# Performance work log

Measured on AMD Instinct MI355X. Metric: run time of the kernel, lower is better.

Reference implementation:

```python
import jax, jax.numpy as jnp
import numpy as np

NEG = -1000000.0  # same finite mask value as the Triton kernel


def setup_inputs() -> dict:
    key = jax.random.key(0)
    k1, k2, k3, k4 = jax.random.split(key, 4)
    B, H, KVH, S, D = 1, 32, 8, 2048, 128
    return {
        "q": jax.random.normal(k1, (B, H, S, D), dtype=jnp.float32),
        "k": jax.random.normal(k2, (B, KVH, S, D), dtype=jnp.float32),
        "v": jax.random.normal(k3, (B, KVH, S, D), dtype=jnp.float32),
        "sinks": jax.random.normal(k4, (H,), dtype=jnp.float32),
        "bandwidth": 1024,
    }


def reference(q, k, v, sinks, bandwidth):
    """Prefill flash attention with causal + sliding-window masking, GQA, and
    per-head attention sinks (extra logit in the softmax denominator)."""
    B, H, S, D = q.shape
    ratio = H // k.shape[1]  # KV_HEAD_RATIO
    kf = jnp.repeat(k, ratio, axis=1)  # [B,H,S,D]
    vf = jnp.repeat(v, ratio, axis=1)
    sm_scale = 1.0 / np.sqrt(D).astype(np.float32)

    logits = jnp.einsum("bhqd,bhkd->bhqk", q, kf) * sm_scale  # [B,H,S,S]
    q_pos = jnp.arange(S)[:, None]
    k_pos = jnp.arange(S)[None, :]
    mask = k_pos > q_pos  # causal
    if bandwidth > 0:
        mask = mask | (k_pos < q_pos - bandwidth + 1)  # sliding window
    logits = jnp.where(mask, NEG, logits)

    sink = sinks[None, :, None]  # [1,H,1] broadcast over batch, query
    m = jnp.maximum(jnp.max(logits, axis=-1), sink)  # [B,H,S]
    p = jnp.exp(logits - m[..., None])
    denom = p.sum(axis=-1) + jnp.exp(sink - m)  # sink contributes to denom only
    out = jnp.einsum("bhqk,bhkd->bhqd", p, vf) / denom[..., None]
    return out
```

## Files before the change

kernel.cpp:

```cpp
#include <hip/hip_runtime.h>
#include <hip/hip_bf16.h>

typedef __bf16 bf16x8 __attribute__((ext_vector_type(8)));
typedef unsigned short u16x8 __attribute__((ext_vector_type(8)));
typedef unsigned int u32x4 __attribute__((ext_vector_type(4)));
typedef float f32x4 __attribute__((ext_vector_type(4)));

#define SLEN 2048
#define DDIM 128
#define NH   32
#define NKVH 8
#define QBLK 128
#define KVB  32
#define KPAD 136
#define VPAD 40
#define PW2  20
#define MINIT  -1e30f
#define MASKED -3e30f

static __device__ __forceinline__ unsigned short f2bfu(float f) {
  union { float f; unsigned u; } x; x.f = f;
  return (unsigned short)((x.u + 0x7fffu + ((x.u >> 16) & 1u)) >> 16);
}
static __device__ __forceinline__ float bfu2f(unsigned short u) {
  union { unsigned u; float f; } x; x.u = ((unsigned)u) << 16;
  return x.f;
}
static __device__ __forceinline__ unsigned cvt_pk_bf16(float lo, float hi) {
  unsigned r;
  asm("v_cvt_pk_bf16_f32 %0, %1, %2" : "=v"(r) : "v"(lo), "v"(hi));
  return r;
}
static __device__ __forceinline__ f32x4 mfma_bf16(u16x8 a, u16x8 b, f32x4 c) {
  return __builtin_amdgcn_mfma_f32_16x16x32_bf16(
      __builtin_bit_cast(bf16x8, a), __builtin_bit_cast(bf16x8, b), c, 0, 0, 0);
}

__global__ __launch_bounds__(256) void conv_kv(const float* __restrict__ k,
                                               const float* __restrict__ v,
                                               unsigned* __restrict__ kdst,
                                               unsigned short* __restrict__ vt) {
  __shared__ unsigned T32[32][17];
  const int bb = blockIdx.x;
  if (bb < 1024) {
    const int i = bb * 256 + threadIdx.x;
    const float4 f0 = ((const float4*)k)[2 * i];
    const float4 f1 = ((const float4*)k)[2 * i + 1];
    u32x4 o = { cvt_pk_bf16(f0.x, f0.y), cvt_pk_bf16(f0.z, f0.w),
                cvt_pk_bf16(f1.x, f1.y), cvt_pk_bf16(f1.z, f1.w) };
    ((u32x4*)kdst)[i] = o;
    return;
  }
  const int b   = bb - 1024;
  const int dt  = b & 3;
  const int st  = (b >> 2) & 63;
  const int kvh = b >> 8;
  const int r  = threadIdx.x >> 3;
  const int cg = threadIdx.x & 7;
  const float4 f = *(const float4*)(v + ((size_t)(kvh * SLEN + st * 32 + r) * DDIM) + dt * 32 + cg * 4);
  T32[r][cg * 2]     = cvt_pk_bf16(f.x, f.y);
  T32[r][cg * 2 + 1] = cvt_pk_bf16(f.z, f.w);
  __syncthreads();
  const int dr = threadIdx.x >> 3;
  const unsigned sel = (dr & 1) ? 0x07060302u : 0x05040100u;
  const unsigned a0 = T32[cg * 4 + 0][dr >> 1], a1 = T32[cg * 4 + 1][dr >> 1];
  const unsigned a2 = T32[cg * 4 + 2][dr >> 1], a3 = T32[cg * 4 + 3][dr >> 1];
  unsigned short* vp = vt + (size_t)kvh * DDIM * SLEN + (size_t)(dt * 32 + dr) * SLEN + st * 32 + cg * 4;
  const unsigned w0 = __builtin_amdgcn_perm(a1, a0, sel);
  const unsigned w1 = __builtin_amdgcn_perm(a3, a2, sel);
  vp[0] = (unsigned short)(w0 & 0xffff);
  vp[1] = (unsigned short)(w0 >> 16);
  vp[2] = (unsigned short)(w1 & 0xffff);
  vp[3] = (unsigned short)(w1 >> 16);
}

__global__ __launch_bounds__(256, 3) void attn_fwd(
    const float* __restrict__ q, const unsigned short* __restrict__ kbf,
    const unsigned short* __restrict__ vtg, const float* __restrict__ sinks,
    const int* __restrict__ bwp, float* __restrict__ out,
    unsigned short* __restrict__ pO, float* __restrict__ pm,
    float* __restrict__ pl, const int nch) {
  __shared__ unsigned short Kl[KVB][KPAD];
  __shared__ unsigned short Vt[DDIM][VPAD];
  __shared__ unsigned Pex[4][2][16][PW2];
  __shared__ float SmS[4][2][16];

  const int tid  = threadIdx.x;
  const int wid  = tid >> 6;
  const int lane = tid & 63;
  const int ln   = lane & 15;
  const int hi   = lane >> 4;

  const int B   = blockIdx.x;
  const int x   = B & 7;
  const int j   = B >> 3;
  const int per = 4 * nch;
  const int qt  = 15 - (j / per);
  const int rem = j % per;
  const int hh  = (nch == 2) ? (rem >> 1) : rem;
  const int c   = (nch == 2) ? (rem & 1) : 0;
  const int h   = x * 4 + hh;
  const int kvh = x;
  const int q0  = qt * QBLK;
  const int qrow0 = q0 + wid * 32;

  const int bwv    = bwp[0];
  const int lo_off = (bwv > 0) ? (bwv - 1) : SLEN;

  const int T0 = max(0, q0 - lo_off) >> 5;
  const int T1 = (q0 + QBLK - 1) >> 5;
  const int N  = T1 - T0 + 1;
  const int ch = (N + nch - 1) / nch;
  const int Ts = T0 + c * ch;
  const int Te = min(T1, Ts + ch - 1);

  const float sm_scale = 0.08838834764831845f;

  u16x8 qf[2][4];
  #pragma unroll
  for (int g = 0; g < 2; ++g) {
    const float* qp = q + ((size_t)(h * SLEN + qrow0 + g * 16 + ln) * DDIM) + hi * 8;
    #pragma unroll
    for (int dk = 0; dk < 4; ++dk) {
      float4 f0 = *(const float4*)(qp + dk * 32);
      float4 f1 = *(const float4*)(qp + dk * 32 + 4);
      u32x4 t = { cvt_pk_bf16(f0.x, f0.y), cvt_pk_bf16(f0.z, f0.w),
                  cvt_pk_bf16(f1.x, f1.y), cvt_pk_bf16(f1.z, f1.w) };
      qf[g][dk] = __builtin_bit_cast(u16x8, t);
    }
  }

  float m[2] = {MINIT, MINIT}, l[2] = {0.0f, 0.0f};
  f32x4 oacc[2][8];
  #pragma unroll
  for (int g = 0; g < 2; ++g)
    #pragma unroll
    for (int nt = 0; nt < 8; ++nt) oacc[g][nt] = f32x4{0.f, 0.f, 0.f, 0.f};

  const unsigned short* Kg = kbf + (size_t)kvh * SLEN * DDIM;
  const unsigned short* Vg = vtg + (size_t)kvh * DDIM * SLEN;

  const int kr0 = tid >> 4,          kc0 = (tid & 15) * 8;
  const int kr1 = (256 + tid) >> 4;
  const int vr0 = tid >> 2,          vc0 = (tid & 3) * 8;
  const int vr1 = (256 + tid) >> 2;

  const int kbS = Ts * 32, kbE = Te * 32;

  u16x8 pk0, pk1, pv0, pv1;
  {
    pk0 = *(const u16x8*)(Kg + (size_t)(kbS + kr0) * DDIM + kc0);
    pk1 = *(const u16x8*)(Kg + (size_t)(kbS + kr1) * DDIM + kc0);
    pv0 = *(const u16x8*)(Vg + (size_t)vr0 * SLEN + kbS + vc0);
    pv1 = *(const u16x8*)(Vg + (size_t)vr1 * SLEN + kbS + vc0);
  }

  for (int kb = kbS; kb <= kbE; kb += KVB) {
    __syncthreads();
    *(u16x8*)&Kl[kr0][kc0] = pk0;
    *(u16x8*)&Kl[kr1][kc0] = pk1;
    *(u16x8*)&Vt[vr0][vc0] = pv0;
    *(u16x8*)&Vt[vr1][vc0] = pv1;
    __syncthreads();

    {
      const int nb = min(kb + KVB, kbE);
      pk0 = *(const u16x8*)(Kg + (size_t)(nb + kr0) * DDIM + kc0);
      pk1 = *(const u16x8*)(Kg + (size_t)(nb + kr1) * DDIM + kc0);
      pv0 = *(const u16x8*)(Vg + (size_t)vr0 * SLEN + nb + vc0);
      pv1 = *(const u16x8*)(Vg + (size_t)vr1 * SLEN + nb + vc0);
    }

    if (kb > qrow0 + 31) continue;
    if (kb + KVB - 1 < qrow0 - lo_off) continue;

    f32x4 s00 = {0,0,0,0}, s01 = {0,0,0,0};
    f32x4 s10 = {0,0,0,0}, s11 = {0,0,0,0};
    #pragma unroll
    for (int dk = 0; dk < 4; ++dk) {
      const u16x8 kf = *(const u16x8*)&Kl[ln][dk*32 + hi*8];
      s00 = mfma_bf16(kf, qf[0][dk], s00);
      s01 = mfma_bf16(kf, qf[1][dk], s01);
    }
    #pragma unroll
    for (int dk = 0; dk < 4; ++dk) {
      const u16x8 kf = *(const u16x8*)&Kl[16 + ln][dk*32 + hi*8];
      s10 = mfma_bf16(kf, qf[0][dk], s10);
      s11 = mfma_bf16(kf, qf[1][dk], s11);
    }

    float p0[8], p1[8];
    const int qpos0 = qrow0 + ln, qpos1 = qrow0 + 16 + ln;
    #pragma unroll
    for (int r = 0; r < 4; ++r) {
      const int kp0 = kb + hi * 4 + r;
      const int kp1 = kp0 + 16;
      p0[r]     = ((kp0 <= qpos0) && (kp0 >= qpos0 - lo_off)) ? s00[r] * sm_scale : MASKED;
      p0[4 + r] = ((kp1 <= qpos0) && (kp1 >= qpos0 - lo_off)) ? s10[r] * sm_scale : MASKED;
      p1[r]     = ((kp0 <= qpos1) && (kp0 >= qpos1 - lo_off)) ? s01[r] * sm_scale : MASKED;
      p1[4 + r] = ((kp1 <= qpos1) && (kp1 >= qpos1 - lo_off)) ? s11[r] * sm_scale : MASKED;
    }

    float mx0 = fmaxf(fmaxf(fmaxf(p0[0], p0[1]), fmaxf(p0[2], p0[3])),
                      fmaxf(fmaxf(p0[4], p0[5]), fmaxf(p0[6], p0[7])));
    float mx1 = fmaxf(fmaxf(fmaxf(p1[0], p1[1]), fmaxf(p1[2], p1[3])),
                      fmaxf(fmaxf(p1[4], p1[5]), fmaxf(p1[6], p1[7])));
    mx0 = fmaxf(mx0, __shfl_xor(mx0, 16));
    mx0 = fmaxf(mx0, __shfl_xor(mx0, 32));
    mx1 = fmaxf(mx1, __shfl_xor(mx1, 16));
    mx1 = fmaxf(mx1, __shfl_xor(mx1, 32));

    if (__any((mx0 > m[0] + 8.0f) || (mx1 > m[1] + 8.0f))) {
      const float mn0 = fmaxf(m[0], mx0), mn1 = fmaxf(m[1], mx1);
      const float c0 = __expf(m[0] - mn0), c1 = __expf(m[1] - mn1);
      l[0] *= c0; l[1] *= c1; m[0] = mn0; m[1] = mn1;
      if (hi == 0) { SmS[wid][0][ln] = c0; SmS[wid][1][ln] = c1; }
      float c40[4], c41[4];
      #pragma unroll
      for (int r = 0; r < 4; ++r) { c40[r] = SmS[wid][0][hi*4 + r]; c41[r] = SmS[wid][1][hi*4 + r]; }
      #pragma unroll
      for (int nt = 0; nt < 8; ++nt)
        #pragma unroll
        for (int r = 0; r < 4; ++r) { oacc[0][nt][r] *= c40[r]; oacc[1][nt][r] *= c41[r]; }
    }

    float s0 = 0.0f, s1 = 0.0f;
    #pragma unroll
    for (int jj = 0; jj < 8; ++jj) {
      p0[jj] = __expf(p0[jj] - m[0]); s0 += p0[jj];
      p1[jj] = __expf(p1[jj] - m[1]); s1 += p1[jj];
    }
    s0 += __shfl_xor(s0, 16); s0 += __shfl_xor(s0, 32); l[0] += s0;
    s1 += __shfl_xor(s1, 16); s1 += __shfl_xor(s1, 32); l[1] += s1;

    Pex[wid][0][ln][hi * 2]         = cvt_pk_bf16(p0[0], p0[1]);
    Pex[wid][0][ln][hi * 2 + 1]     = cvt_pk_bf16(p0[2], p0[3]);
    Pex[wid][0][ln][8 + hi * 2]     = cvt_pk_bf16(p0[4], p0[5]);
    Pex[wid][0][ln][8 + hi * 2 + 1] = cvt_pk_bf16(p0[6], p0[7]);
    Pex[wid][1][ln][hi * 2]         = cvt_pk_bf16(p1[0], p1[1]);
    Pex[wid][1][ln][hi * 2 + 1]     = cvt_pk_bf16(p1[2], p1[3]);
    Pex[wid][1][ln][8 + hi * 2]     = cvt_pk_bf16(p1[4], p1[5]);
    Pex[wid][1][ln][8 + hi * 2 + 1] = cvt_pk_bf16(p1[6], p1[7]);
    const u16x8 pa0 = __builtin_bit_cast(u16x8, *(const u32x4*)&Pex[wid][0][ln][hi * 4]);
    const u16x8 pa1 = __builtin_bit_cast(u16x8, *(const u32x4*)&Pex[wid][1][ln][hi * 4]);

    #pragma unroll
    for (int nt = 0; nt < 8; ++nt) {
      const u16x8 vb = *(const u16x8*)&Vt[nt*16 + ln][hi*8];
      oacc[0][nt] = mfma_bf16(pa0, vb, oacc[0][nt]);
      oacc[1][nt] = mfma_bf16(pa1, vb, oacc[1][nt]);
    }
  }

  if (nch == 1) {
    const float sink = sinks[h];
    #pragma unroll
    for (int g = 0; g < 2; ++g) {
      const float M  = fmaxf(m[g], sink);
      const float ed = __expf(m[g] - M);
      const float fac_ln = ed / (l[g] * ed + __expf(sink - M));
      if (hi == 0) SmS[wid][g][ln] = fac_ln;
      float fac4[4];
      #pragma unroll
      for (int r = 0; r < 4; ++r) fac4[r] = SmS[wid][g][hi * 4 + r];
      #pragma unroll
      for (int r = 0; r < 4; ++r) {
        float* op = out + ((size_t)(h * SLEN + qrow0 + g*16 + hi*4 + r) * DDIM) + ln;
        #pragma unroll
        for (int nt = 0; nt < 8; ++nt) op[nt * 16] = oacc[g][nt][r] * fac4[r];
      }
    }
  } else {
    const size_t Lb = ((size_t)(h * 16 + qt)) * 2 + c;
    #pragma unroll
    for (int g = 0; g < 2; ++g) {
      if (hi == 0) {
        pm[Lb * 128 + wid * 32 + g * 16 + ln] = m[g];
        pl[Lb * 128 + wid * 32 + g * 16 + ln] = l[g];
      }
      #pragma unroll
      for (int r = 0; r < 4; ++r) {
        unsigned short* po = pO + (Lb * 128 + wid * 32 + g * 16 + hi * 4 + r) * 128 + ln;
        #pragma unroll
        for (int nt = 0; nt < 8; ++nt) po[nt * 16] = f2bfu(oacc[g][nt][r]);
      }
    }
  }
}

__global__ __launch_bounds__(256) void merge2(
    const unsigned short* __restrict__ pO, const float* __restrict__ pm,
    const float* __restrict__ pl, const float* __restrict__ sinks,
    float* __restrict__ out) {
  const int blk  = blockIdx.x;
  const int h    = blk >> 5;
  const int rloc = (blk & 31) * 64 + (threadIdx.x >> 2);
  const int d0   = (threadIdx.x & 3) * 32;
  const int qt   = rloc >> 7;
  const int lr   = rloc & 127;
  const size_t r0 = ((size_t)((h * 16 + qt) * 2 + 0)) * 128 + lr;
  const size_t r1 = r0 + 128;
  const float m0 = pm[r0], l0 = pl[r0];
  const float m1 = pm[r1], l1 = pl[r1];
  const float sink = sinks[h];
  const float M  = fmaxf(fmaxf(m0, m1), sink);
  const float e0 = __expf(m0 - M), e1 = __expf(m1 - M);
  const float inv = 1.0f / (l0 * e0 + l1 * e1 + __expf(sink - M));
  const float s0 = e0 * inv, s1 = e1 * inv;
  const unsigned short* p0 = pO + r0 * 128 + d0;
  const unsigned short* p1 = pO + r1 * 128 + d0;
  float* op = out + ((size_t)h * SLEN + rloc) * DDIM + d0;
  #pragma unroll
  for (int i = 0; i < 4; ++i) {
    u16x8 a = *(const u16x8*)(p0 + i * 8);
    u16x8 b = *(const u16x8*)(p1 + i * 8);
    float4 o0, o1;
    o0.x = bfu2f(a[0]) * s0 + bfu2f(b[0]) * s1;
    o0.y = bfu2f(a[1]) * s0 + bfu2f(b[1]) * s1;
    o0.z = bfu2f(a[2]) * s0 + bfu2f(b[2]) * s1;
    o0.w = bfu2f(a[3]) * s0 + bfu2f(b[3]) * s1;
    o1.x = bfu2f(a[4]) * s0 + bfu2f(b[4]) * s1;
    o1.y = bfu2f(a[5]) * s0 + bfu2f(b[5]) * s1;
    o1.z = bfu2f(a[6]) * s0 + bfu2f(b[6]) * s1;
    o1.w = bfu2f(a[7]) * s0 + bfu2f(b[7]) * s1;
    *(float4*)(op + i * 8)     = o0;
    *(float4*)(op + i * 8 + 4) = o1;
  }
}

extern "C" void kernel_launch(void* const* d_in, const int* in_sizes, int n_in,
                              void* d_out, int out_size, void* d_ws, size_t ws_size,
                              hipStream_t stream) {
  const float* q     = (const float*)d_in[0];
  const float* k     = (const float*)d_in[1];
  const float* v     = (const float*)d_in[2];
  const float* sinks = (const float*)d_in[3];
  const int*   bw    = (const int*)d_in[4];
  float* out = (float*)d_out;

  const size_t kvBytes = (size_t)NKVH * SLEN * DDIM * 2;
  unsigned short* kbf = (unsigned short*)d_ws;
  unsigned short* vtg = kbf + (size_t)NKVH * SLEN * DDIM;

  const size_t nPart   = (size_t)NH * 16 * 2 * 128;
  const size_t oBytes  = nPart * 128 * 2;
  const size_t mlBytes = nPart * 4 * 2;
  const size_t need2   = 2 * kvBytes + oBytes + mlBytes;

  const int nch = (ws_size >= need2) ? 2 : 1;

  unsigned short* pO = vtg + (size_t)NKVH * SLEN * DDIM;
  float* pm = (float*)((char*)pO + oBytes);
  float* pl = pm + nPart;

  conv_kv<<<dim3(1024 + NKVH * 64 * 4), 256, 0, stream>>>(k, v, (unsigned*)kbf, vtg);
  attn_fwd<<<dim3(512 * nch), 256, 0, stream>>>(q, kbf, vtg, sinks, bw, out,
                                                pO, pm, pl, nch);
  if (nch == 2)
    merge2<<<dim3(1024), 256, 0, stream>>>(pO, pm, pl, sinks, out);
}
```

Measured before the change: 86.84 us.

## Template attention kernel on query groups and KV splits, add 4-way split path

The attention kernel is templated on the number of 16-row query groups per wave and the number of KV-range chunks. The default path (large workspace) splits each query tile's KV range into 4 chunks, launching 2048 blocks instead of 1024. A generic N-way merge kernel combines the partials. Fallbacks use 64-row query tiles with 2 chunks, or no split. This raises parallelism and load balance across CUs, at the cost of more partial-output traffic in bf16 and a heavier merge.

Result: slower. 109.2 us (+25.7%).

```diff
diff --git a/kernel.cpp b/kernel.cpp
--- a/kernel.cpp
+++ b/kernel.cpp
@@ -10,7 +10,6 @@
 #define DDIM 128
 #define NH   32
 #define NKVH 8
-#define QBLK 128
 #define KVB  32
 #define KPAD 136
 #define VPAD 40
@@ -74,16 +73,19 @@
   vp[3] = (unsigned short)(w1 >> 16);
 }
 
-__global__ __launch_bounds__(256, 3) void attn_fwd(
+template <int NG, int NCH>
+__global__ __launch_bounds__(256, NG == 1 ? 4 : 3) void attn_fwd(
     const float* __restrict__ q, const unsigned short* __restrict__ kbf,
     const unsigned short* __restrict__ vtg, const float* __restrict__ sinks,
     const int* __restrict__ bwp, float* __restrict__ out,
     unsigned short* __restrict__ pO, float* __restrict__ pm,
-    float* __restrict__ pl, const int nch) {
+    float* __restrict__ pl) {
+  constexpr int QBLK = 64 * NG;
+  constexpr int NQT  = SLEN / QBLK;
   __shared__ unsigned short Kl[KVB][KPAD];
   __shared__ unsigned short Vt[DDIM][VPAD];
-  __shared__ unsigned Pex[4][2][16][PW2];
-  __shared__ float SmS[4][2][16];
+  __shared__ unsigned Pex[4][16][PW2];
+  __shared__ float SmS[4][NG][16];
 
   const int tid  = threadIdx.x;
   const int wid  = tid >> 6;
@@ -94,15 +96,15 @@
   const int B   = blockIdx.x;
   const int x   = B & 7;
   const int j   = B >> 3;
-  const int per = 4 * nch;
-  const int qt  = 15 - (j / per);
+  constexpr int per = 4 * NCH;
+  const int qt  = NQT - 1 - (j / per);
   const int rem = j % per;
-  const int hh  = (nch == 2) ? (rem >> 1) : rem;
-  const int c   = (nch == 2) ? (rem & 1) : 0;
+  const int hh  = rem / NCH;
+  const int c   = rem % NCH;
   const int h   = x * 4 + hh;
   const int kvh = x;
   const int q0  = qt * QBLK;
-  const int qrow0 = q0 + wid * 32;
+  const int qrow0 = q0 + wid * (16 * NG);
 
   const int bwv    = bwp[0];
   const int lo_off = (bwv > 0) ? (bwv - 1) : SLEN;
@@ -110,15 +112,15 @@
   const int T0 = max(0, q0 - lo_off) >> 5;
   const int T1 = (q0 + QBLK - 1) >> 5;
   const int N  = T1 - T0 + 1;
-  const int ch = (N + nch - 1) / nch;
+  const int ch = (N + NCH - 1) / NCH;
   const int Ts = T0 + c * ch;
   const int Te = min(T1, Ts + ch - 1);
 
   const float sm_scale = 0.08838834764831845f;
 
-  u16x8 qf[2][4];
-  #pragma unroll
-  for (int g = 0; g < 2; ++g) {
+  u16x8 qf[NG][4];
+  #pragma unroll
+  for (int g = 0; g < NG; ++g) {
     const float* qp = q + ((size_t)(h * SLEN + qrow0 + g * 16 + ln) * DDIM) + hi * 8;
     #pragma unroll
     for (int dk = 0; dk < 4; ++dk) {
@@ -130,12 +132,14 @@
     }
   }
 
-  float m[2] = {MINIT, MINIT}, l[2] = {0.0f, 0.0f};
-  f32x4 oacc[2][8];
-  #pragma unroll
-  for (int g = 0; g < 2; ++g)
+  float m[NG], l[NG];
+  f32x4 oacc[NG][8];
+  #pragma unroll
+  for (int g = 0; g < NG; ++g) {
+    m[g] = MINIT; l[g] = 0.0f;
     #pragma unroll
     for (int nt = 0; nt < 8; ++nt) oacc[g][nt] = f32x4{0.f, 0.f, 0.f, 0.f};
+  }
 
   const unsigned short* Kg = kbf + (size_t)kvh * SLEN * DDIM;
   const unsigned short* Vg = vtg + (size_t)kvh * DDIM * SLEN;
@@ -145,117 +149,131 @@
   const int vr0 = tid >> 2,          vc0 = (tid & 3) * 8;
   const int vr1 = (256 + tid) >> 2;
 
-  const int kbS = Ts * 32, kbE = Te * 32;
-
-  u16x8 pk0, pk1, pv0, pv1;
-  {
-    pk0 = *(const u16x8*)(Kg + (size_t)(kbS + kr0) * DDIM + kc0);
-    pk1 = *(const u16x8*)(Kg + (size_t)(kbS + kr1) * DDIM + kc0);
-    pv0 = *(const u16x8*)(Vg + (size_t)vr0 * SLEN + kbS + vc0);
-    pv1 = *(const u16x8*)(Vg + (size_t)vr1 * SLEN + kbS + vc0);
-  }
-
-  for (int kb = kbS; kb <= kbE; kb += KVB) {
-    __syncthreads();
-    *(u16x8*)&Kl[kr0][kc0] = pk0;
-    *(u16x8*)&Kl[kr1][kc0] = pk1;
-    *(u16x8*)&Vt[vr0][vc0] = pv0;
-    *(u16x8*)&Vt[vr1][vc0] = pv1;
-    __syncthreads();
-
+  if (Ts <= Te) {
+    const int kbS = Ts * 32, kbE = Te * 32;
+
+    u16x8 pk0, pk1, pv0, pv1;
     {
-      const int nb = min(kb + KVB, kbE);
-      pk0 = *(const u16x8*)(Kg + (size_t)(nb + kr0) * DDIM + kc0);
-      pk1 = *(const u16x8*)(Kg + (size_t)(nb + kr1) * DDIM + kc0);
-      pv0 = *(const u16x8*)(Vg + (size_t)vr0 * SLEN + nb + vc0);
-      pv1 = *(const u16x8*)(Vg + (size_t)vr1 * SLEN + nb + vc0);
-    }
-
-    if (kb > qrow0 + 31) continue;
-    if (kb + KVB - 1 < qrow0 - lo_off) continue;
-
-    f32x4 s00 = {0,0,0,0}, s01 = {0,0,0,0};
-    f32x4 s10 = {0,0,0,0}, s11 = {0,0,0,0};
-    #pragma unroll
-    for (int dk = 0; dk < 4; ++dk) {
-      const u16x8 kf = *(const u16x8*)&Kl[ln][dk*32 + hi*8];
-      s00 = mfma_bf16(kf, qf[0][dk], s00);
-      s01 = mfma_bf16(kf, qf[1][dk], s01);
-    }
-    #pragma unroll
-    for (int dk = 0; dk < 4; ++dk) {
-      const u16x8 kf = *(const u16x8*)&Kl[16 + ln][dk*32 + hi*8];
-      s10 = mfma_bf16(kf, qf[0][dk], s10);
-      s11 = mfma_bf16(kf, qf[1][dk], s11);
-    }
-
-    float p0[8], p1[8];
-    const int qpos0 = qrow0 + ln, qpos1 = qrow0 + 16 + ln;
-    #pragma unroll
-    for (int r = 0; r < 4; ++r) {
-      const int kp0 = kb + hi * 4 + r;
-      const int kp1 = kp0 + 16;
-      p0[r]     = ((kp0 <= qpos0) && (kp0 >= qpos0 - lo_off)) ? s00[r] * sm_scale : MASKED;
-      p0[4 + r] = ((kp1 <= qpos0) && (kp1 >= qpos0 - lo_off)) ? s10[r] * sm_scale : MASKED;
-      p1[r]     = ((kp0 <= qpos1) && (kp0 >= qpos1 - lo_off)) ? s01[r] * sm_scale : MASKED;
-      p1[4 + r] = ((kp1 <= qpos1) && (kp1 >= qpos1 - lo_off)) ? s11[r] * sm_scale : MASKED;
-    }
-
-    float mx0 = fmaxf(fmaxf(fmaxf(p0[0], p0[1]), fmaxf(p0[2], p0[3])),
-                      fmaxf(fmaxf(p0[4], p0[5]), fmaxf(p0[6], p0[7])));
-    float mx1 = fmaxf(fmaxf(fmaxf(p1[0], p1[1]), fmaxf(p1[2], p1[3])),
-                      fmaxf(fmaxf(p1[4], p1[5]), fmaxf(p1[6], p1[7])));
-    mx0 = fmaxf(mx0, __shfl_xor(mx0, 16));
-    mx0 = fmaxf(mx0, __shfl_xor(mx0, 32));
-    mx1 = fmaxf(mx1, __shfl_xor(mx1, 16));
-    mx1 = fmaxf(mx1, __shfl_xor(mx1, 32));
-
-    if (__any((mx0 > m[0] + 8.0f) || (mx1 > m[1] + 8.0f))) {
-      const float mn0 = fmaxf(m[0], mx0), mn1 = fmaxf(m[1], mx1);
-      const float c0 = __expf(m[0] - mn0), c1 = __expf(m[1] - mn1);
-      l[0] *= c0; l[1] *= c1; m[0] = mn0; m[1] = mn1;
-      if (hi == 0) { SmS[wid][0][ln] = c0; SmS[wid][1][ln] = c1; }
-      float c40[4], c41[4];
-      #pragma unroll
-      for (int r = 0; r < 4; ++r) { c40[r] = SmS[wid][0][hi*4 + r]; c41[r] = SmS[wid][1][hi*4 + r]; }
-      #pragma unroll
-      for (int nt = 0; nt < 8; ++nt)
-        #pragma unroll
-        for (int r = 0; r < 4; ++r) { oacc[0][nt][r] *= c40[r]; oacc[1][nt][r] *= c41[r]; }
-    }
-
-    float s0 = 0.0f, s1 = 0.0f;
-    #pragma unroll
-    for (int jj = 0; jj < 8; ++jj) {
-      p0[jj] = __expf(p0[jj] - m[0]); s0 += p0[jj];
-      p1[jj] = __expf(p1[jj] - m[1]); s1 += p1[jj];
-    }
-    s0 += __shfl_xor(s0, 16); s0 += __shfl_xor(s0, 32); l[0] += s0;
-    s1 += __shfl_xor(s1, 16); s1 += __shfl_xor(s1, 32); l[1] += s1;
-
-    Pex[wid][0][ln][hi * 2]         = cvt_pk_bf16(p0[0], p0[1]);
-    Pex[wid][0][ln][hi * 2 + 1]     = cvt_pk_bf16(p0[2], p0[3]);
-    Pex[wid][0][ln][8 + hi * 2]     = cvt_pk_bf16(p0[4], p0[5]);
-    Pex[wid][0][ln][8 + hi * 2 + 1] = cvt_pk_bf16(p0[6], p0[7]);
-    Pex[wid][1][ln][hi * 2]         = cvt_pk_bf16(p1[0], p1[1]);
-    Pex[wid][1][ln][hi * 2 + 1]     = cvt_pk_bf16(p1[2], p1[3]);
-    Pex[wid][1][ln][8 + hi * 2]     = cvt_pk_bf16(p1[4], p1[5]);
-    Pex[wid][1][ln][8 + hi * 2 + 1] = cvt_pk_bf16(p1[6], p1[7]);
-    const u16x8 pa0 = __builtin_bit_cast(u16x8, *(const u32x4*)&Pex[wid][0][ln][hi * 4]);
-    const u16x8 pa1 = __builtin_bit_cast(u16x8, *(const u32x4*)&Pex[wid][1][ln][hi * 4]);
-
-    #pragma unroll
-    for (int nt = 0; nt < 8; ++nt) {
-      const u16x8 vb = *(const u16x8*)&Vt[nt*16 + ln][hi*8];
-      oacc[0][nt] = mfma_bf16(pa0, vb, oacc[0][nt]);
-      oacc[1][nt] = mfma_bf16(pa1, vb, oacc[1][nt]);
-    }
-  }
-
-  if (nch == 1) {
+      pk0 = *(const u16x8*)(Kg + (size_t)(kbS + kr0) * DDIM + kc0);
+      pk1 = *(const u16x8*)(Kg + (size_t)(kbS + kr1) * DDIM + kc0);
+      pv0 = *(const u16x8*)(Vg + (size_t)vr0 * SLEN + kbS + vc0);
+      pv1 = *(const u16x8*)(Vg + (size_t)vr1 * SLEN + kbS + vc0);
+    }
+
+    for (int kb = kbS; kb <= kbE; kb += KVB) {
+      __syncthreads();
+      *(u16x8*)&Kl[kr0][kc0] = pk0;
+      *(u16x8*)&Kl[kr1][kc0] = pk1;
+      *(u16x8*)&Vt[vr0][vc0] = pv0;
+      *(u16x8*)&Vt[vr1][vc0] = pv1;
+      __syncthreads();
+
+      {
+        const int nb = min(kb + KVB, kbE);
+        pk0 = *(const u16x8*)(Kg + (size_t)(nb + kr0) * DDIM + kc0);
+        pk1 = *(const u16x8*)(Kg + (size_t)(nb + kr1) * DDIM + kc0);
+        pv0 = *(const u16x8*)(Vg + (size_t)vr0 * SLEN + nb + vc0);
+        pv1 = *(const u16x8*)(Vg + (size_t)vr1 * SLEN + nb + vc0);
+      }
+
+      if (kb > qrow0 + 16 * NG - 1) continue;
+      if (kb + KVB - 1 < qrow0 - lo_off) continue;
+
+      f32x4 sA[NG], sB[NG];
+      #pragma unroll
+      for (int g = 0; g < NG; ++g) { sA[g] = f32x4{0,0,0,0}; sB[g] = f32x4{0,0,0,0}; }
+      #pragma unroll
+      for (int dk = 0; dk < 4; ++dk) {
+        const u16x8 kf = *(const u16x8*)&Kl[ln][dk*32 + hi*8];
+        #pragma unroll
+        for (int g = 0; g < NG; ++g) sA[g] = mfma_bf16(kf, qf[g][dk], sA[g]);
+      }
+      #pragma unroll
+      for (int dk = 0; dk < 4; ++dk) {
+        const u16x8 kf = *(const u16x8*)&Kl[16 + ln][dk*32 + hi*8];
+        #pragma unroll
+        for (int g = 0; g < NG; ++g) sB[g] = mfma_bf16(kf, qf[g][dk], sB[g]);
+      }
+
+      float p[NG][8];
+      #pragma unroll
+      for (int g = 0; g < NG; ++g) {
+        const int qpos = qrow0 + g * 16 + ln;
+        #pragma unroll
+        for (int r = 0; r < 4; ++r) {
+          const int kp0 = kb + hi * 4 + r;
+          const int kp1 = kp0 + 16;
+          p[g][r]     = ((kp0 <= qpos) && (kp0 >= qpos - lo_off)) ? sA[g][r] * sm_scale : MASKED;
+          p[g][4 + r] = ((kp1 <= qpos) && (kp1 >= qpos - lo_off)) ? sB[g][r] * sm_scale : MASKED;
+        }
+      }
+
+      float mx[NG];
+      bool need = false;
+      #pragma unroll
+      for (int g = 0; g < NG; ++g) {
+        float t = fmaxf(fmaxf(fmaxf(p[g][0], p[g][1]), fmaxf(p[g][2], p[g][3])),
+                        fmaxf(fmaxf(p[g][4], p[g][5]), fmaxf(p[g][6], p[g][7])));
+        t = fmaxf(t, __shfl_xor(t, 16));
+        t = fmaxf(t, __shfl_xor(t, 32));
+        mx[g] = t;
+        need = need || (t > m[g] + 8.0f);
+      }
+
+      if (__any(need)) {
+        float corr[NG];
+        #pragma unroll
+        for (int g = 0; g < NG; ++g) {
+          const float mn = fmaxf(m[g], mx[g]);
+          corr[g] = __expf(m[g] - mn);
+          l[g] *= corr[g];
+          m[g] = mn;
+          if (hi == 0) SmS[wid][g][ln] = corr[g];
+        }
+        #pragma unroll
+        for (int g = 0; g < NG; ++g) {
+          float c4[4];
+          #pragma unroll
+          for (int r = 0; r < 4; ++r) c4[r] = SmS[wid][g][hi * 4 + r];
+          #pragma unroll
+          for (int nt = 0; nt < 8; ++nt)
+            #pragma unroll
+            for (int r = 0; r < 4; ++r) oacc[g][nt][r] *= c4[r];
+        }
+      }
+
+      #pragma unroll
+      for (int g = 0; g < NG; ++g) {
+        float s = 0.0f;
+        #pragma unroll
+        for (int jj = 0; jj < 8; ++jj) { p[g][jj] = __expf(p[g][jj] - m[g]); s += p[g][jj]; }
+        s += __shfl_xor(s, 16);
+        s += __shfl_xor(s, 32);
+        l[g] += s;
+      }
+
+      u16x8 pa[NG];
+      #pragma unroll
+      for (int g = 0; g < NG; ++g) {
+        Pex[wid][ln][hi * 2]         = cvt_pk_bf16(p[g][0], p[g][1]);
+        Pex[wid][ln][hi * 2 + 1]     = cvt_pk_bf16(p[g][2], p[g][3]);
+        Pex[wid][ln][8 + hi * 2]     = cvt_pk_bf16(p[g][4], p[g][5]);
+        Pex[wid][ln][8 + hi * 2 + 1] = cvt_pk_bf16(p[g][6], p[g][7]);
+        pa[g] = __builtin_bit_cast(u16x8, *(const u32x4*)&Pex[wid][ln][hi * 4]);
+      }
+      #pragma unroll
+      for (int nt = 0; nt < 8; ++nt) {
+        const u16x8 vb = *(const u16x8*)&Vt[nt*16 + ln][hi*8];
+        #pragma unroll
+        for (int g = 0; g < NG; ++g) oacc[g][nt] = mfma_bf16(pa[g], vb, oacc[g][nt]);
+      }
+    }
+  }
+
+  if (NCH == 1) {
     const float sink = sinks[h];
     #pragma unroll
-    for (int g = 0; g < 2; ++g) {
+    for (int g = 0; g < NG; ++g) {
       const float M  = fmaxf(m[g], sink);
       const float ed = __expf(m[g] - M);
       const float fac_ln = ed / (l[g] * ed + __expf(sink - M));
@@ -271,16 +289,17 @@
       }
     }
   } else {
-    const size_t Lb = ((size_t)(h * 16 + qt)) * 2 + c;
-    #pragma unroll
-    for (int g = 0; g < 2; ++g) {
+    const size_t Lb = ((size_t)(h * NQT + qt)) * NCH + c;
+    #pragma unroll
+    for (int g = 0; g < NG; ++g) {
+      const int rbase = wid * (16 * NG) + g * 16;
       if (hi == 0) {
-        pm[Lb * 128 + wid * 32 + g * 16 + ln] = m[g];
-        pl[Lb * 128 + wid * 32 + g * 16 + ln] = l[g];
+        pm[Lb * QBLK + rbase + ln] = m[g];
+        pl[Lb * QBLK + rbase + ln] = l[g];
       }
       #pragma unroll
       for (int r = 0; r < 4; ++r) {
-        unsigned short* po = pO + (Lb * 128 + wid * 32 + g * 16 + hi * 4 + r) * 128 + ln;
+        unsigned short* po = pO + (Lb * QBLK + rbase + hi * 4 + r) * 128 + ln;
         #pragma unroll
         for (int nt = 0; nt < 8; ++nt) po[nt * 16] = f2bfu(oacc[g][nt][r]);
       }
@@ -288,44 +307,51 @@
   }
 }
 
-__global__ __launch_bounds__(256) void merge2(
+template <int NCH, int QBLK, int NQT>
+__global__ __launch_bounds__(256) void mergeN(
     const unsigned short* __restrict__ pO, const float* __restrict__ pm,
     const float* __restrict__ pl, const float* __restrict__ sinks,
     float* __restrict__ out) {
-  const int blk  = blockIdx.x;
-  const int h    = blk >> 5;
-  const int rloc = (blk & 31) * 64 + (threadIdx.x >> 2);
-  const int d0   = (threadIdx.x & 3) * 32;
-  const int qt   = rloc >> 7;
-  const int lr   = rloc & 127;
-  const size_t r0 = ((size_t)((h * 16 + qt) * 2 + 0)) * 128 + lr;
-  const size_t r1 = r0 + 128;
-  const float m0 = pm[r0], l0 = pl[r0];
-  const float m1 = pm[r1], l1 = pl[r1];
+  const int t    = blockIdx.x * 256 + threadIdx.x;
+  const int rid  = t >> 2;
+  const int d0   = (t & 3) * 32;
+  const int h    = rid >> 11;
+  const int qpos = rid & 2047;
+  const int qt   = qpos / QBLK;
+  const int lr   = qpos % QBLK;
+  const size_t base = ((size_t)(h * NQT + qt) * NCH) * QBLK + lr;
   const float sink = sinks[h];
-  const float M  = fmaxf(fmaxf(m0, m1), sink);
-  const float e0 = __expf(m0 - M), e1 = __expf(m1 - M);
-  const float inv = 1.0f / (l0 * e0 + l1 * e1 + __expf(sink - M));
-  const float s0 = e0 * inv, s1 = e1 * inv;
-  const unsigned short* p0 = pO + r0 * 128 + d0;
-  const unsigned short* p1 = pO + r1 * 128 + d0;
-  float* op = out + ((size_t)h * SLEN + rloc) * DDIM + d0;
-  #pragma unroll
-  for (int i = 0; i < 4; ++i) {
-    u16x8 a = *(const u16x8*)(p0 + i * 8);
-    u16x8 b = *(const u16x8*)(p1 + i * 8);
-    float4 o0, o1;
-    o0.x = bfu2f(a[0]) * s0 + bfu2f(b[0]) * s1;
-    o0.y = bfu2f(a[1]) * s0 + bfu2f(b[1]) * s1;
-    o0.z = bfu2f(a[2]) * s0 + bfu2f(b[2]) * s1;
-    o0.w = bfu2f(a[3]) * s0 + bfu2f(b[3]) * s1;
-    o1.x = bfu2f(a[4]) * s0 + bfu2f(b[4]) * s1;
-    o1.y = bfu2f(a[5]) * s0 + bfu2f(b[5]) * s1;
-    o1.z = bfu2f(a[6]) * s0 + bfu2f(b[6]) * s1;
-    o1.w = bfu2f(a[7]) * s0 + bfu2f(b[7]) * s1;
-    *(float4*)(op + i * 8)     = o0;
-    *(float4*)(op + i * 8 + 4) = o1;
-  }
+  float mc[NCH], lc[NCH];
+  float M = sink;
+  #pragma unroll
+  for (int c = 0; c < NCH; ++c) {
+    mc[c] = pm[base + (size_t)c * QBLK];
+    lc[c] = pl[base + (size_t)c * QBLK];
+    M = fmaxf(M, mc[c]);
+  }
+  float denom = __expf(sink - M);
+  float sc[NCH];
+  #pragma unroll
+  for (int c = 0; c < NCH; ++c) { sc[c] = __expf(mc[c] - M); denom += lc[c] * sc[c]; }
+  const float inv = 1.0f / denom;
+  float o[32];
+  #pragma unroll
+  for (int i = 0; i < 32; ++i) o[i] = 0.f;
+  #pragma unroll
+  for (int c = 0; c < NCH; ++c) {
+    const unsigned short* pp = pO + (base + (size_t)c * QBLK) * 128 + d0;
+    const float s = sc[c] * inv;
+    #pragma unroll
+    for (int i = 0; i < 4; ++i) {
+      u16x8 a = *(const u16x8*)(pp + i * 8);
+      #pragma unroll
+      for (int jj = 0; jj < 8; ++jj) o[i*8+jj] += bfu2f(a[jj]) * s;
+    }
+  }
+  float* op = out + (size_t)rid * 128 + d0;
+  #pragma unroll
+  for (int i = 0; i < 8; ++i)
+    *(float4*)(op + i*4) = make_float4(o[i*4], o[i*4+1], o[i*4+2], o[i*4+3]);
 }
 
 extern "C" void kernel_launch(void* const* d_in, const int* in_sizes, int n_in,
@@ -338,24 +364,29 @@
   const int*   bw    = (const int*)d_in[4];
   float* out = (float*)d_out;
 
-  const size_t kvBytes = (size_t)NKVH * SLEN * DDIM * 2;
+  const size_t kvElems = (size_t)NKVH * SLEN * DDIM;
   unsigned short* kbf = (unsigned short*)d_ws;
-  unsigned short* vtg = kbf + (size_t)NKVH * SLEN * DDIM;
-
-  const size_t nPart   = (size_t)NH * 16 * 2 * 128;
-  const size_t oBytes  = nPart * 128 * 2;
-  const size_t mlBytes = nPart * 4 * 2;
-  const size_t need2   = 2 * kvBytes + oBytes + mlBytes;
-
-  const int nch = (ws_size >= need2) ? 2 : 1;
-
-  unsigned short* pO = vtg + (size_t)NKVH * SLEN * DDIM;
-  float* pm = (float*)((char*)pO + oBytes);
-  float* pl = pm + nPart;
+  unsigned short* vtg = kbf + kvElems;
+  unsigned short* pO  = vtg + kvElems;
+
+  const size_t nPart4 = (size_t)NH * 16 * 4 * 128;
+  const size_t need4  = 4 * kvElems + nPart4 * 128 * 2 + nPart4 * 8;
+  const size_t nPart2 = (size_t)NH * 32 * 2 * 64;
+  const size_t need2  = 4 * kvElems + nPart2 * 128 * 2 + nPart2 * 8;
 
   conv_kv<<<dim3(1024 + NKVH * 64 * 4), 256, 0, stream>>>(k, v, (unsigned*)kbf, vtg);
-  attn_fwd<<<dim3(512 * nch), 256, 0, stream>>>(q, kbf, vtg, sinks, bw, out,
-                                                pO, pm, pl, nch);
-  if (nch == 2)
-    merge2<<<dim3(1024), 256, 0, stream>>>(pO, pm, pl, sinks, out);
-}
+
+  if (ws_size >= need4) {
+    float* pm = (float*)(pO + nPart4 * 128);
+    float* pl = pm + nPart4;
+    attn_fwd<2, 4><<<dim3(2048), 256, 0, stream>>>(q, kbf, vtg, sinks, bw, out, pO, pm, pl);
+    mergeN<4, 128, 16><<<dim3(1024), 256, 0, stream>>>(pO, pm, pl, sinks, out);
+  } else if (ws_size >= need2) {
+    float* pm = (float*)(pO + nPart2 * 128);
+    float* pl = pm + nPart2;
+    attn_fwd<1, 2><<<dim3(2048), 256, 0, stream>>>(q, kbf, vtg, sinks, bw, out, pO, pm, pl);
+    mergeN<2, 64, 32><<<dim3(1024), 256, 0, stream>>>(pO, pm, pl, sinks, out);
+  } else {
+    attn_fwd<1, 1><<<dim3(1024), 256, 0, stream>>>(q, kbf, vtg, sinks, bw, out, pO, nullptr, nullptr);
+  }
+}
```
